# Optimization experiments

Measured on AMD Instinct MI355X. Metric: run time of the kernel, lower is better.

Reference implementation:

```python
import jax, jax.numpy as jnp
import numpy as np
from jax import lax

B, N, C = 4, 4096, 512
NUM_HEADS = 8
HD = C // NUM_HEADS  # 64, equals L
L = 64               # H = W = L, N = L*L


def setup_inputs() -> dict:
    key = jax.random.key(0)
    ks = jax.random.split(key, 8)
    d = HD
    return {
        "x": jax.random.normal(ks[0], (B, N, C), jnp.float32),
        "log_peak_width": jnp.log(jnp.float32(3.0)),
        "log_valley_width": jnp.log(jnp.float32(3.0)),
        "w_qkv": jax.random.normal(ks[1], (3 * C, C), jnp.float32) * 0.02,
        "b_qkv": jnp.zeros((3 * C,), jnp.float32),
        "w_proj": jax.random.normal(ks[2], (C, C), jnp.float32) * 0.02,
        "b_proj": jnp.zeros((C,), jnp.float32),
        "omega": jnp.linspace(0.1, 10.0, d // 2).astype(jnp.float32),
        "w_pp1": jax.random.normal(ks[3], (2 * d, 1, 3), jnp.float32) * 0.3,   # grouped conv, groups=d
        "b_pp1": jnp.zeros((2 * d,), jnp.float32),
        "w_pp2": jax.random.normal(ks[4], (d, 2 * d, 1), jnp.float32) * 0.1,
        "b_pp2": jnp.zeros((d,), jnp.float32),
        "w_gate": jax.random.normal(ks[5], (d, d, 1), jnp.float32) * 0.1,
        "b_gate": jnp.zeros((d,), jnp.float32),
    }


def _spectral_gate(x_spec, log_pw, log_vw):
    # x_spec: [B, C, N]. torch nonzero flattens (b,c,i) -> use per-position counts
    # (exactly equivalent to summing one gaussian per nonzero occurrence).
    n = x_spec.shape[-1]
    sc = jnp.sign(jnp.diff(jnp.diff(x_spec, axis=-1), axis=-1))       # [B,C,N-2]
    peak_cnt = jnp.sum(sc < 0, axis=(0, 1)).astype(x_spec.dtype)      # [N-2]
    valley_cnt = jnp.sum(sc > 0, axis=(0, 1)).astype(x_spec.dtype)    # [N-2]
    pos = jnp.arange(n, dtype=x_spec.dtype)
    centers = jnp.arange(1, n - 1, dtype=x_spec.dtype)                # index i+1

    def gsum(cnt, logw):
        dist = (pos[None, :] - centers[:, None]) * jnp.exp(-logw)     # [N-2, N]
        return cnt @ jnp.exp(-dist * dist)                            # [N]

    attn = gsum(peak_cnt, log_pw) + gsum(valley_cnt, log_vw)
    return (attn - attn.min()) / (attn.max() - attn.min() + 1e-6)     # [N], uniform over (B,C)


def _spectral_pe(omega, w1, b1, w2, b2, wg, bg, l, d):
    grid = jnp.arange(l, dtype=jnp.float32)
    rel = grid[:, None] - grid[None, :]                               # [l,l]
    freqs = rel[..., None] * omega                                    # [l,l,d/2]
    pe = jnp.concatenate([jnp.sin(freqs), jnp.cos(freqs)], axis=-1)   # [l,l,d]
    pe = pe.reshape(l * l, d).T[None]                                 # [1,d,l*l]
    dn = ('NCH', 'OIH', 'NCH')
    h = lax.conv_general_dilated(pe, w1, (1,), [(1, 1)], dimension_numbers=dn,
                                 feature_group_count=d) + b1[None, :, None]
    h = jax.nn.gelu(h, approximate=False)
    pe2 = (lax.conv_general_dilated(h, w2, (1,), [(0, 0)],
                                    dimension_numbers=dn) + b2[None, :, None])[0]  # [d, l*l]
    gate = jax.nn.sigmoid(wg[:, :, 0] @ pe2.mean(-1, keepdims=True) + bg[:, None])  # [d,1]
    pe3 = pe2.T.reshape(l, l, d)
    # torch rearrange '(l1 l2) d -> l1 l2 d' on [d,1] gate: reshape to [l, d//l, 1] and broadcast
    return pe3 * gate.reshape(l, d // l, 1)


def _rope(t, pe, d):
    b, h, n, _ = t.shape
    l = pe.shape[0]
    tr = t.reshape(b, h, l, l, d)
    tr = tr + tr * pe * (d ** -0.25)
    return tr.reshape(b, h, n, d)


def reference(x, log_peak_width, log_valley_width, w_qkv, b_qkv, w_proj, b_proj,
              omega, w_pp1, b_pp1, w_pp2, b_pp2, w_gate, b_gate):
    b, n, c = x.shape
    h, d = NUM_HEADS, HD
    gate = _spectral_gate(x.transpose(0, 2, 1), log_peak_width, log_valley_width)  # [n]
    xg = x * gate[None, :, None]
    qkv = xg @ w_qkv.T + b_qkv                                        # [b,n,3c]
    q, k, v = jnp.split(qkv, 3, axis=-1)
    tohead = lambda t: t.reshape(b, n, h, d).transpose(0, 2, 1, 3)    # [b,h,n,d]
    q, k, v = tohead(q), tohead(k), tohead(v)
    q = jax.nn.elu(q) + 1.0
    k = jax.nn.elu(k) + 1.0
    pe = _spectral_pe(omega, w_pp1, b_pp1, w_pp2, b_pp2, w_gate, b_gate, L, d)
    q = _rope(q, pe, d)
    k = _rope(k, pe, d)
    scale = (d * n) ** -0.5
    ctx = jnp.einsum('bhnd,bhne->bhde', q, k) * scale                 # [b,h,d,d]
    out = jnp.einsum('bhnd,bhde->bhne', v, ctx) * scale               # [b,h,n,d]
    out = out.transpose(0, 2, 1, 3).reshape(b, n, c)
    return out @ w_proj.T + b_proj
```

## Files before the change

kernel.cpp:

```cpp
#include <hip/hip_runtime.h>
#include <hip/hip_bf16.h>
#include <math.h>

constexpr int BB = 4;
constexpr int NN = 4096;
constexpr int CC = 512;
constexpr int HH = 8;
constexpr int DD = 64;
constexpr int NCNT = NN - 2;

typedef __bf16 bf16x8 __attribute__((ext_vector_type(8)));
typedef float f32x4 __attribute__((ext_vector_type(4)));

__device__ __forceinline__ float b2f(ushort u) {
  unsigned v = ((unsigned)u) << 16;
  return __builtin_bit_cast(float, v);
}
__device__ __forceinline__ ushort f2b(float f) {
  __hip_bfloat16 h = __float2bfloat16(f);
  return __builtin_bit_cast(ushort, h);
}
__device__ __forceinline__ void gload16(const ushort* g, ushort* l) {
  __builtin_amdgcn_global_load_lds(
      (const __attribute__((address_space(1))) unsigned int*)g,
      (__attribute__((address_space(3))) unsigned int*)l, 16, 0, 0);
}

__global__ __launch_bounds__(512) void k_counts_prep(
    const float* __restrict__ x, int* __restrict__ pcntP,
    int* __restrict__ pcntV, ushort* __restrict__ Xh) {
  int b = blockIdx.x >> 8;
  int tile = blockIdx.x & 255;
  int c = threadIdx.x;
  int lane = threadIdx.x & 63;
  int i0 = tile * 16;
  const float* xb = x + (size_t)b * NN * CC + c;

  float v[18];
  #pragma unroll
  for (int r = 0; r < 18; ++r) {
    int i = i0 + r;
    v[r] = xb[(size_t)(i < NN ? i : NN - 1) * CC];
  }

  #pragma unroll
  for (int r = 0; r < 16; ++r)
    Xh[((size_t)b * NN + i0 + r) * CC + c] = f2b(v[r]);

  __shared__ int redP[16], redV[16];
  if (threadIdx.x < 16) { redP[threadIdx.x] = 0; redV[threadIdx.x] = 0; }
  __syncthreads();

  #pragma unroll
  for (int r = 0; r < 16; ++r) {
    int i = i0 + r;
    if (i < NCNT) {
      float d2 = (v[r + 2] - v[r + 1]) - (v[r + 1] - v[r]);
      unsigned long long mneg = __ballot(d2 < 0.0f);
      unsigned long long mpos = __ballot(d2 > 0.0f);
      if (lane == 0) {
        atomicAdd(&redP[r], __popcll(mneg));
        atomicAdd(&redV[r], __popcll(mpos));
      }
    }
  }
  __syncthreads();
  if (threadIdx.x < 16) {
    int i = i0 + threadIdx.x;
    pcntP[b * NN + i] = (i < NCNT) ? redP[threadIdx.x] : 0;
    pcntV[b * NN + i] = (i < NCNT) ? redV[threadIdx.x] : 0;
  }
}

__global__ void k_etab2(const float* __restrict__ lpw, const float* __restrict__ lvw,
                        const int* __restrict__ pcntP, const int* __restrict__ pcntV,
                        float* __restrict__ etabP, float* __restrict__ etabV,
                        float* __restrict__ fcntP, float* __restrict__ fcntV) {
  int i = blockIdx.x * 256 + threadIdx.x;
  float ipw = expf(-lpw[0]);
  float ivw = expf(-lvw[0]);
  float t1 = (float)i * ipw;
  float t2 = (float)i * ivw;
  etabP[i] = expf(-t1 * t1);
  etabV[i] = expf(-t2 * t2);
  fcntP[i] = (float)(pcntP[i] + pcntP[NN + i] + pcntP[2 * NN + i] + pcntP[3 * NN + i]);
  fcntV[i] = (float)(pcntV[i] + pcntV[NN + i] + pcntV[2 * NN + i] + pcntV[3 * NN + i]);
}

__global__ void k_gsum(const float* __restrict__ fcntP, const float* __restrict__ fcntV,
                       const float* __restrict__ etabP, const float* __restrict__ etabV,
                       float* __restrict__ attn) {
  int p = blockIdx.x;
  int tid = threadIdx.x;
  float acc = 0.f;
  for (int i = tid; i < NCNT; i += 256) {
    int a = p - 1 - i;
    a = a < 0 ? -a : a;
    acc += fcntP[i] * etabP[a] + fcntV[i] * etabV[a];
  }
  __shared__ float red[256];
  red[tid] = acc;
  __syncthreads();
  for (int s = 128; s > 0; s >>= 1) {
    if (tid < s) red[tid] += red[tid + s];
    __syncthreads();
  }
  if (tid == 0) attn[p] = red[0];
}

__global__ void k_norm(const float* __restrict__ attn, float* __restrict__ gate) {
  int tid = threadIdx.x;
  float v0 = attn[tid], v1 = attn[tid + 1024], v2 = attn[tid + 2048], v3 = attn[tid + 3072];
  float mn = fminf(fminf(v0, v1), fminf(v2, v3));
  float mx = fmaxf(fmaxf(v0, v1), fmaxf(v2, v3));
  __shared__ float rmn[1024], rmx[1024];
  rmn[tid] = mn; rmx[tid] = mx;
  __syncthreads();
  for (int s = 512; s > 0; s >>= 1) {
    if (tid < s) {
      rmn[tid] = fminf(rmn[tid], rmn[tid + s]);
      rmx[tid] = fmaxf(rmx[tid], rmx[tid + s]);
    }
    __syncthreads();
  }
  float lo = rmn[0];
  float denom = rmx[0] - rmn[0] + 1e-6f;
  gate[tid]        = (v0 - lo) / denom;
  gate[tid + 1024] = (v1 - lo) / denom;
  gate[tid + 2048] = (v2 - lo) / denom;
  gate[tid + 3072] = (v3 - lo) / denom;
}

__global__ __launch_bounds__(256) void k_pe(
    const float* __restrict__ omega,
    const float* __restrict__ w1, const float* __restrict__ b1,
    const float* __restrict__ w2, const float* __restrict__ b2,
    float* __restrict__ pe2) {
  int g = threadIdx.x >> 6;
  int j = threadIdx.x & 63;
  int n = blockIdx.x * 4 + g;
  __shared__ float pec[4][3][64];
  __shared__ float hs[4][128];
  for (int t = 0; t < 3; ++t) {
    int m = n + t - 1;
    float v = 0.f;
    if (m >= 0 && m < NN) {
      int l1 = m >> 6, l2 = m & 63;
      float rel = (float)(l1 - l2);
      v = (j < 32) ? sinf(rel * omega[j]) : cosf(rel * omega[j - 32]);
    }
    pec[g][t][j] = v;
  }
  __syncthreads();
  for (int o = j; o < 128; o += 64) {
    int ci = o >> 1;
    float hv = b1[o];
    #pragma unroll
    for (int t = 0; t < 3; ++t) hv += pec[g][t][ci] * w1[o * 3 + t];
    hv = 0.5f * hv * (1.f + erff(hv * 0.70710678118654752f));
    hs[g][o] = hv;
  }
  __syncthreads();
  float acc = b2[j];
  for (int o = 0; o < 128; ++o) acc += hs[g][o] * w2[j * 128 + o];
  pe2[(size_t)j * NN + n] = acc;
}

__global__ void k_gatepe(const float* __restrict__ pe2,
                         const float* __restrict__ wg, const float* __restrict__ bg,
                         float* __restrict__ gpe) {
  int tid = threadIdx.x;
  int j = tid & 63, part = tid >> 6;
  float s = 0.f;
  const float* row = pe2 + (size_t)j * NN + part * 1024;
  for (int t = 0; t < 1024; ++t) s += row[t];
  __shared__ float ps[4][64];
  __shared__ float mean[64];
  ps[part][j] = s;
  __syncthreads();
  if (tid < 64) mean[j] = (ps[0][j] + ps[1][j] + ps[2][j] + ps[3][j]) * (1.f / 4096.f);
  __syncthreads();
  if (tid < 64) {
    float g = bg[j];
    for (int k2 = 0; k2 < 64; ++k2) g += wg[j * 64 + k2] * mean[k2];
    gpe[j] = 1.f / (1.f + expf(-g));
  }
}

__global__ void k_ropemul(const float* __restrict__ pe2, const float* __restrict__ gpe,
                          float* __restrict__ ropem) {
  int idx = blockIdx.x * 256 + threadIdx.x;
  int n = idx >> 6, dd = idx & 63;
  ropem[idx] = 1.f + pe2[(size_t)dd * NN + n] * gpe[n >> 6] * 0.35355339059327373f;
}

__global__ void k_prep_h(const float* __restrict__ src,
                         ushort* __restrict__ Sh, int nelem) {
  int idx4 = (blockIdx.x * 256 + threadIdx.x) * 4;
  if (idx4 >= nelem) return;
  float4 v = *(const float4*)&src[idx4];
  ushort4 h;
  ((ushort*)&h)[0] = f2b(v.x);
  ((ushort*)&h)[1] = f2b(v.y);
  ((ushort*)&h)[2] = f2b(v.z);
  ((ushort*)&h)[3] = f2b(v.w);
  *(ushort4*)&Sh[idx4] = h;
}

__global__ __launch_bounds__(256) void k_prep_wvt(const float* __restrict__ wqkv,
                                                  ushort* __restrict__ Wvth,
                                                  ushort* __restrict__ Wvtl) {
  int bx = blockIdx.x & 7;
  int by = blockIdx.x >> 3;
  __shared__ float t[64][65];
  int tid = threadIdx.x;
  #pragma unroll
  for (int it = 0; it < 4; ++it) {
    int idx = tid + it * 256;
    int r = idx >> 4;
    int c4 = (idx & 15) * 4;
    float4 v = *(const float4*)&wqkv[(size_t)(1024 + by * 64 + r) * 512 + bx * 64 + c4];
    t[r][c4] = v.x; t[r][c4 + 1] = v.y; t[r][c4 + 2] = v.z; t[r][c4 + 3] = v.w;
  }
  __syncthreads();
  #pragma unroll
  for (int it = 0; it < 4; ++it) {
    int idx = tid + it * 256;
    int r = idx >> 4;
    int c4 = (idx & 15) * 4;
    ushort4 h4, l4;
    #pragma unroll
    for (int q = 0; q < 4; ++q) {
      float v = t[c4 + q][r];
      ushort hi = f2b(v);
      ((ushort*)&h4)[q] = hi;
      ((ushort*)&l4)[q] = f2b(v - b2f(hi));
    }
    size_t o = (size_t)(bx * 64 + r) * 512 + by * 64 + c4;
    *(ushort4*)&Wvth[o] = h4;
    *(ushort4*)&Wvtl[o] = l4;
  }
}

template <int BN, int EPI>
__global__ __launch_bounds__(512) void k_gemm8(
    const ushort* __restrict__ Ag, const ushort* __restrict__ Bgh,
    const float* __restrict__ bias, const float* __restrict__ gate,
    const float* __restrict__ ropem,
    float* __restrict__ outF, ushort* __restrict__ qT, ushort* __restrict__ kT,
    int ntn, int ncols) {
  constexpr int NF = BN / 32;
  constexpr int BCH = BN / 16;
  const int nwg = gridDim.x;
  const int hw = blockIdx.x;
  const int logical = (hw & 7) * (nwg >> 3) + (hw >> 3);
  const int m0 = (logical / ntn) * 256, n0 = (logical % ntn) * BN;

  const int tid = threadIdx.x, wave = tid >> 6, lane = tid & 63;
  const int wm = wave >> 1, wn = wave & 1;
  __shared__ ushort sA[2][8192];
  __shared__ ushort sB[2][BN * 32];
  f32x4 acc[4][NF] = {};

  const int lr = lane >> 2;
  const int ci = lane & 3;
  const int scol = (ci ^ ((lr >> 1) & 3)) * 8;
  const int rA = lane & 15;
  const int cswz = ((lane >> 4) ^ ((rA >> 1) & 3)) * 8;

  const ushort* pA0 = Ag + (size_t)(m0 + (2 * wave) * 16 + lr) * CC + scol;
  const ushort* pA1 = Ag + (size_t)(m0 + (2 * wave + 1) * 16 + lr) * CC + scol;
  const ushort* Bh_ = Bgh + (EPI == 2 ? (size_t)(m0 >> 12) * 262144 : 0);
  const ushort* pB0 = Bh_ + (size_t)(n0 + wave * 16 + lr) * CC + scol;

#define STAGE(T, S)                                                        \
  {                                                                        \
    gload16(pA0 + (T) * 32, &sA[S][(2 * wave) * 512]);                     \
    gload16(pA1 + (T) * 32, &sA[S][(2 * wave + 1) * 512]);                 \
    if (BCH == 8) {                                                        \
      gload16(pB0 + (T) * 32, &sB[S][wave * 512]);                         \
    } else {                                                               \
      if (wave < BCH) gload16(pB0 + (T) * 32, &sB[S][wave * 512]);         \
    }                                                                      \
  }

  STAGE(0, 0);
  __syncthreads();

  #pragma unroll
  for (int t = 0; t < 16; ++t) {
    if (t < 15) STAGE(t + 1, (t + 1) & 1);
    const int cur = t & 1;
    bf16x8 af[4], bhf[NF];
    #pragma unroll
    for (int m = 0; m < 4; ++m)
      af[m] = *(const bf16x8*)(&sA[cur][(wm * 64 + m * 16 + rA) * 32 + cswz]);
    #pragma unroll
    for (int n = 0; n < NF; ++n)
      bhf[n] = *(const bf16x8*)(&sB[cur][(wn * (BN / 2) + n * 16 + rA) * 32 + cswz]);
    #pragma unroll
    for (int m = 0; m < 4; ++m)
      #pragma unroll
      for (int n = 0; n < NF; ++n)
        acc[m][n] = __builtin_amdgcn_mfma_f32_16x16x32_bf16(af[m], bhf[n], acc[m][n], 0, 0, 0);
    __syncthreads();
  }
#undef STAGE

  const int kj = lane >> 4, l15 = lane & 15;
  #pragma unroll
  for (int m = 0; m < 4; ++m) {
    #pragma unroll
    for (int n = 0; n < NF; ++n) {
      if (EPI == 2) {
        #pragma unroll
        for (int r = 0; r < 4; ++r) {
          int row = m0 + wm * 64 + m * 16 + kj * 4 + r;
          int col = n0 + wn * (BN / 2) + n * 16 + l15;
          int nseq = row & (NN - 1), b = row >> 12;
          float val = acc[m][n][r] * gate[nseq] + bias[b * 512 + col];
          outF[(size_t)row * ncols + col] = val;
        }
      } else {
        int rowb = m0 + wm * 64 + m * 16 + kj * 4;
        int col = n0 + wn * (BN / 2) + n * 16 + l15;
        int nseqb = rowb & (NN - 1), b = rowb >> 12;
        int part = col >> 9, h = (col >> 6) & 7, dd = col & 63;
        ushort4 pk;
        #pragma unroll
        for (int r = 0; r < 4; ++r) {
          int nseq = nseqb + r;
          float val = acc[m][n][r] * gate[nseq] + bias[col];
          float e = val > 0.f ? val + 1.f : expf(val);
          ((ushort*)&pk)[r] = f2b(e * ropem[nseq * 64 + dd]);
        }
        ushort* dst = (part == 0 ? qT : kT) +
                      ((size_t)(b * HH + h) * DD + dd) * NN + nseqb;
        *(ushort4*)dst = pk;
      }
    }
  }
}

__global__ __launch_bounds__(256) void k_gemm_g2(
    const ushort* __restrict__ Ag, const ushort* __restrict__ Bgh,
    const ushort* __restrict__ Bgl, ushort* __restrict__ outB, int ntn) {
  const int nwg = gridDim.x;
  const int hw = blockIdx.x;
  const int logical = (hw & 7) * (nwg >> 3) + (hw >> 3);
  const int m0 = (logical / ntn) * 128, n0 = (logical % ntn) * 128;

  const int tid = threadIdx.x, wave = tid >> 6, lane = tid & 63;
  const int wm = wave >> 1, wn = wave & 1;
  __shared__ ushort sA[2][4096];
  __shared__ ushort sB[2][8192];
  f32x4 acc[4][4] = {};

  const int lr = lane >> 2;
  const int ci = lane & 3;
  const int scol = (ci ^ ((lr >> 1) & 3)) * 8;
  const int rA = lane & 15;
  const int cswz = ((lane >> 4) ^ ((rA >> 1) & 3)) * 8;

  const int chunk0 = wave * 2, chunk1 = wave * 2 + 1;
  const ushort* pA0 = Ag + (size_t)(m0 + chunk0 * 16 + lr) * CC + scol;
  const ushort* pA1 = Ag + (size_t)(m0 + chunk1 * 16 + lr) * CC + scol;
  const ushort* pB0 = Bgh + (size_t)(n0 + chunk0 * 16 + lr) * CC + scol;
  const ushort* pB1 = Bgh + (size_t)(n0 + chunk1 * 16 + lr) * CC + scol;
  const ushort* pB0l = Bgl + (size_t)(n0 + chunk0 * 16 + lr) * CC + scol;
  const ushort* pB1l = Bgl + (size_t)(n0 + chunk1 * 16 + lr) * CC + scol;

#define STAGE(T, S)                                                        \
  {                                                                        \
    gload16(pA0 + (T) * 32, &sA[S][chunk0 * 512]);                         \
    gload16(pA1 + (T) * 32, &sA[S][chunk1 * 512]);                         \
    gload16(pB0 + (T) * 32, &sB[S][chunk0 * 512]);                         \
    gload16(pB1 + (T) * 32, &sB[S][chunk1 * 512]);                         \
    gload16(pB0l + (T) * 32, &sB[S][4096 + chunk0 * 512]);                 \
    gload16(pB1l + (T) * 32, &sB[S][4096 + chunk1 * 512]);                 \
  }

  STAGE(0, 0);
  __syncthreads();

  #pragma unroll
  for (int t = 0; t < 16; ++t) {
    if (t < 15) STAGE(t + 1, (t + 1) & 1);
    const int cur = t & 1;
    bf16x8 af[4], bh[4], bl[4];
    #pragma unroll
    for (int m = 0; m < 4; ++m)
      af[m] = *(const bf16x8*)(&sA[cur][(wm * 64 + m * 16 + rA) * 32 + cswz]);
    #pragma unroll
    for (int n = 0; n < 4; ++n) {
      int off = (wn * 64 + n * 16 + rA) * 32 + cswz;
      bh[n] = *(const bf16x8*)(&sB[cur][off]);
      bl[n] = *(const bf16x8*)(&sB[cur][4096 + off]);
    }
    #pragma unroll
    for (int m = 0; m < 4; ++m)
      #pragma unroll
      for (int n = 0; n < 4; ++n) {
        acc[m][n] = __builtin_amdgcn_mfma_f32_16x16x32_bf16(af[m], bh[n], acc[m][n], 0, 0, 0);
        acc[m][n] = __builtin_amdgcn_mfma_f32_16x16x32_bf16(af[m], bl[n], acc[m][n], 0, 0, 0);
      }
    __syncthreads();
  }
#undef STAGE

  const int kj = lane >> 4, l15 = lane & 15;
  #pragma unroll
  for (int m = 0; m < 4; ++m)
    #pragma unroll
    for (int n = 0; n < 4; ++n)
      #pragma unroll
      for (int r = 0; r < 4; ++r) {
        int row = m0 + wm * 64 + m * 16 + kj * 4 + r;
        int col = n0 + wn * 64 + n * 16 + l15;
        outB[(size_t)row * 512 + col] = f2b(acc[m][n][r]);
      }
}

__global__ __launch_bounds__(256) void k_ctx_mfma(
    const ushort* __restrict__ qT, const ushort* __restrict__ kT,
    float* __restrict__ ctxp) {
  int blk = blockIdx.x;
  int bh = blk >> 4, chunk = blk & 15;
  int wave = threadIdx.x >> 6, lane = threadIdx.x & 63;
  int l15 = lane & 15, kj = lane >> 4;
  const size_t base = (size_t)bh * DD * NN;
  const int n0 = chunk * 256 + wave * 64;
  f32x4 acc[4][4] = {};
  #pragma unroll
  for (int ks = 0; ks < 2; ++ks) {
    const int nb = n0 + ks * 32 + kj * 8;
    bf16x8 qa[4], ka[4];
    #pragma unroll
    for (int m = 0; m < 4; ++m)
      qa[m] = *(const bf16x8*)(qT + base + (size_t)(m * 16 + l15) * NN + nb);
    #pragma unroll
    for (int n = 0; n < 4; ++n)
      ka[n] = *(const bf16x8*)(kT + base + (size_t)(n * 16 + l15) * NN + nb);
    #pragma unroll
    for (int m = 0; m < 4; ++m)
      #pragma unroll
      for (int n = 0; n < 4; ++n)
        acc[m][n] = __builtin_amdgcn_mfma_f32_16x16x32_bf16(qa[m], ka[n], acc[m][n], 0, 0, 0);
  }
  __shared__ float red[4][4096];
  #pragma unroll
  for (int m = 0; m < 4; ++m)
    #pragma unroll
    for (int n = 0; n < 4; ++n)
      #pragma unroll
      for (int r = 0; r < 4; ++r)
        red[wave][(m * 16 + kj * 4 + r) * 64 + n * 16 + l15] = acc[m][n][r];
  __syncthreads();
  const float scale = 1.f / 512.f;
  float* dst = ctxp + (size_t)(bh * 16 + chunk) * 4096;
  #pragma unroll
  for (int e = 0; e < 16; ++e) {
    int idx = threadIdx.x + e * 256;
    float s = red[0][idx] + red[1][idx] + red[2][idx] + red[3][idx];
    dst[idx] = s * scale;
  }
}

__global__ void k_ctx_red(const float* __restrict__ ctxp, float* __restrict__ ctx) {
  int idx = blockIdx.x * 256 + threadIdx.x;
  int bh = idx >> 12, off = idx & 4095;
  float s = 0.f;
  #pragma unroll
  for (int c2 = 0; c2 < 16; ++c2)
    s += ctxp[((size_t)bh * 16 + c2) * 4096 + off];
  ctx[idx] = s;
}

__global__ __launch_bounds__(256) void k_mproj(
    const float* __restrict__ ctx, const float* __restrict__ wp,
    ushort* __restrict__ Mfh, ushort* __restrict__ Mfl) {
  int blk = blockIdx.x;
  int b = blk >> 6, h = (blk >> 3) & 7, oq = blk & 7;
  int tid = threadIdx.x;
  int o = oq * 64 + (tid & 63);
  int d0 = (tid >> 6) * 16;
  __shared__ float cs[64][64];
  #pragma unroll
  for (int it = 0; it < 4; ++it) {
    int idx = (tid + 256 * it) * 4;
    *(float4*)&cs[idx >> 6][idx & 63] =
        *(const float4*)&ctx[(size_t)(b * 8 + h) * 4096 + idx];
  }
  __syncthreads();
  float wv[64];
  #pragma unroll
  for (int e = 0; e < 64; ++e) wv[e] = wp[(size_t)o * 512 + h * 64 + e];
  for (int d = d0; d < d0 + 16; ++d) {
    float s = 0.f;
    #pragma unroll
    for (int e = 0; e < 64; ++e) s += cs[d][e] * wv[e];
    s *= (1.f / 512.f);
    ushort hi = f2b(s);
    size_t idx = ((size_t)b * 512 + o) * 512 + h * 64 + d;
    Mfh[idx] = hi;
    Mfl[idx] = f2b(s - b2f(hi));
  }
}

__global__ void k_beff(const ushort* __restrict__ Mfh, const ushort* __restrict__ Mfl,
                       const float* __restrict__ bqkv,
                       const float* __restrict__ bproj, float* __restrict__ beff) {
  int w = threadIdx.x >> 6, lane = threadIdx.x & 63;
  int t = blockIdx.x * 4 + w;
  int b = t >> 9, o = t & 511;
  size_t base = ((size_t)b * 512 + o) * 512;
  float s = 0.f;
  #pragma unroll
  for (int c = 0; c < 512; c += 64) {
    float m = b2f(Mfh[base + c + lane]) + b2f(Mfl[base + c + lane]);
    s += bqkv[1024 + c + lane] * m;
  }
  #pragma unroll
  for (int off = 32; off > 0; off >>= 1) s += __shfl_down(s, off);
  if (lane == 0) beff[t] = s + bproj[o];
}

extern "C" void kernel_launch(void* const* d_in, const int* in_sizes, int n_in,
                              void* d_out, int out_size, void* d_ws, size_t ws_size,
                              hipStream_t stream) {
  const float* x    = (const float*)d_in[0];
  const float* lpw  = (const float*)d_in[1];
  const float* lvw  = (const float*)d_in[2];
  const float* wqkv = (const float*)d_in[3];
  const float* bqkv = (const float*)d_in[4];
  const float* wproj= (const float*)d_in[5];
  const float* bproj= (const float*)d_in[6];
  const float* omega= (const float*)d_in[7];
  const float* w1   = (const float*)d_in[8];
  const float* b1   = (const float*)d_in[9];
  const float* w2   = (const float*)d_in[10];
  const float* b2   = (const float*)d_in[11];
  const float* wg   = (const float*)d_in[12];
  const float* bg   = (const float*)d_in[13];
  float* out = (float*)d_out;

  constexpr size_t MB = 1024 * 1024;
  char* w = (char*)d_ws;
  int*   pcntP  = (int*)(w);
  int*   pcntV  = (int*)(w + 64 * 1024);
  float* attn   = (float*)(w + 128 * 1024);
  float* gate   = (float*)(w + 144 * 1024);
  float* etabP  = (float*)(w + 160 * 1024);
  float* etabV  = (float*)(w + 176 * 1024);
  float* fcntP  = (float*)(w + 192 * 1024);
  float* fcntV  = (float*)(w + 208 * 1024);
  float* pe2    = (float*)(w + 256 * 1024);
  float* gpe    = (float*)(w + 1280 * 1024);
  float* ropem  = (float*)(w + 1344 * 1024);
  ushort* Xh    = (ushort*)(w + 4 * MB);
  ushort* qT    = (ushort*)(w + 20 * MB);
  ushort* kT    = (ushort*)(w + 36 * MB);
  ushort* Whqk  = (ushort*)(w + 52 * MB);
  ushort* Wvth  = (ushort*)(w + 53 * MB);
  ushort* Wvtl  = (ushort*)(w + 53 * MB + 512 * 1024);
  ushort* Mfh   = (ushort*)(w + 54 * MB);
  ushort* Mfl   = (ushort*)(w + 56 * MB);
  ushort* G2h   = (ushort*)(w + 58 * MB);
  float* beff   = (float*)(w + 60 * MB);
  float* ctxp   = (float*)(w + 61 * MB);
  float* ctx    = (float*)(w + 69 * MB);

  k_counts_prep<<<BB * 256, 512, 0, stream>>>(x, pcntP, pcntV, Xh);
  k_etab2<<<16, 256, 0, stream>>>(lpw, lvw, pcntP, pcntV, etabP, etabV, fcntP, fcntV);
  k_gsum<<<NN, 256, 0, stream>>>(fcntP, fcntV, etabP, etabV, attn);
  k_norm<<<1, 1024, 0, stream>>>(attn, gate);
  k_pe<<<1024, 256, 0, stream>>>(omega, w1, b1, w2, b2, pe2);
  k_gatepe<<<1, 256, 0, stream>>>(pe2, wg, bg, gpe);
  k_ropemul<<<1024, 256, 0, stream>>>(pe2, gpe, ropem);
  k_prep_h<<<512, 256, 0, stream>>>(wqkv, Whqk, 1024 * CC);
  k_prep_wvt<<<64, 256, 0, stream>>>(wqkv, Wvth, Wvtl);

  k_gemm8<128, 1><<<512, 512, 0, stream>>>(Xh, Whqk, bqkv, gate, ropem,
                                           nullptr, qT, kT, 8, 0);
  k_ctx_mfma<<<512, 256, 0, stream>>>(qT, kT, ctxp);
  k_ctx_red<<<512, 256, 0, stream>>>(ctxp, ctx);
  k_mproj<<<256, 256, 0, stream>>>(ctx, wproj, Mfh, Mfl);
  k_gemm_g2<<<64, 256, 0, stream>>>(Mfh, Wvth, Wvtl, G2h, 4);
  k_beff<<<512, 256, 0, stream>>>(Mfh, Mfl, bqkv, bproj, beff);

  k_gemm8<64, 2><<<512, 512, 0, stream>>>(Xh, G2h, beff, gate, nullptr,
                                          out, nullptr, nullptr, 8, 512);
}
```

Measured before the change: 178.7 us.

## Merge independent small kernels into block-dispatched combined launches

Independent preprocessing kernels (counts/bf16 cast, positional-encoding MLP, weight casts and transpose) are fused into one launch that dispatches on block index. The gate-table and PE-mean, the gsum and rope-multiplier, and the G2 GEMM and effective-bias kernels are likewise paired into shared launches. This cuts the launch count from 15 to 9, removing launch gaps and letting independent work run concurrently. In exchange the fused kernels share one register and LDS budget sized for the heaviest branch, which can reduce occupancy for the lighter branches.

```diff
diff --git a/kernel.cpp b/kernel.cpp
--- a/kernel.cpp
+++ b/kernel.cpp
@@ -26,86 +26,205 @@
       (__attribute__((address_space(3))) unsigned int*)l, 16, 0, 0);
 }
 
-__global__ __launch_bounds__(512) void k_counts_prep(
+__global__ __launch_bounds__(512) void k_front(
     const float* __restrict__ x, int* __restrict__ pcntP,
-    int* __restrict__ pcntV, ushort* __restrict__ Xh) {
-  int b = blockIdx.x >> 8;
-  int tile = blockIdx.x & 255;
-  int c = threadIdx.x;
-  int lane = threadIdx.x & 63;
-  int i0 = tile * 16;
-  const float* xb = x + (size_t)b * NN * CC + c;
-
-  float v[18];
-  #pragma unroll
-  for (int r = 0; r < 18; ++r) {
-    int i = i0 + r;
-    v[r] = xb[(size_t)(i < NN ? i : NN - 1) * CC];
-  }
-
-  #pragma unroll
-  for (int r = 0; r < 16; ++r)
-    Xh[((size_t)b * NN + i0 + r) * CC + c] = f2b(v[r]);
-
-  __shared__ int redP[16], redV[16];
-  if (threadIdx.x < 16) { redP[threadIdx.x] = 0; redV[threadIdx.x] = 0; }
-  __syncthreads();
-
-  #pragma unroll
-  for (int r = 0; r < 16; ++r) {
-    int i = i0 + r;
-    if (i < NCNT) {
-      float d2 = (v[r + 2] - v[r + 1]) - (v[r + 1] - v[r]);
-      unsigned long long mneg = __ballot(d2 < 0.0f);
-      unsigned long long mpos = __ballot(d2 > 0.0f);
-      if (lane == 0) {
-        atomicAdd(&redP[r], __popcll(mneg));
-        atomicAdd(&redV[r], __popcll(mpos));
+    int* __restrict__ pcntV, ushort* __restrict__ Xh,
+    const float* __restrict__ omega,
+    const float* __restrict__ w1, const float* __restrict__ b1,
+    const float* __restrict__ w2, const float* __restrict__ b2,
+    float* __restrict__ pe2,
+    const float* __restrict__ wqkv, ushort* __restrict__ Whqk,
+    ushort* __restrict__ Wvth, ushort* __restrict__ Wvtl) {
+  __shared__ __attribute__((aligned(16))) char sm[16896];
+  const int blk = blockIdx.x;
+  const int tid = threadIdx.x;
+
+  if (blk < 1024) {
+    int b = blk >> 8;
+    int tile = blk & 255;
+    int c = tid;
+    int lane = tid & 63;
+    int i0 = tile * 16;
+    const float* xb = x + (size_t)b * NN * CC + c;
+
+    float v[18];
+    #pragma unroll
+    for (int r = 0; r < 18; ++r) {
+      int i = i0 + r;
+      v[r] = xb[(size_t)(i < NN ? i : NN - 1) * CC];
+    }
+    #pragma unroll
+    for (int r = 0; r < 16; ++r)
+      Xh[((size_t)b * NN + i0 + r) * CC + c] = f2b(v[r]);
+
+    int* redP = (int*)sm;
+    int* redV = redP + 16;
+    if (tid < 16) { redP[tid] = 0; redV[tid] = 0; }
+    __syncthreads();
+    #pragma unroll
+    for (int r = 0; r < 16; ++r) {
+      int i = i0 + r;
+      if (i < NCNT) {
+        float d2 = (v[r + 2] - v[r + 1]) - (v[r + 1] - v[r]);
+        unsigned long long mneg = __ballot(d2 < 0.0f);
+        unsigned long long mpos = __ballot(d2 > 0.0f);
+        if (lane == 0) {
+          atomicAdd(&redP[r], __popcll(mneg));
+          atomicAdd(&redV[r], __popcll(mpos));
+        }
       }
     }
-  }
-  __syncthreads();
-  if (threadIdx.x < 16) {
-    int i = i0 + threadIdx.x;
-    pcntP[b * NN + i] = (i < NCNT) ? redP[threadIdx.x] : 0;
-    pcntV[b * NN + i] = (i < NCNT) ? redV[threadIdx.x] : 0;
-  }
-}
-
-__global__ void k_etab2(const float* __restrict__ lpw, const float* __restrict__ lvw,
-                        const int* __restrict__ pcntP, const int* __restrict__ pcntV,
-                        float* __restrict__ etabP, float* __restrict__ etabV,
-                        float* __restrict__ fcntP, float* __restrict__ fcntV) {
-  int i = blockIdx.x * 256 + threadIdx.x;
-  float ipw = expf(-lpw[0]);
-  float ivw = expf(-lvw[0]);
-  float t1 = (float)i * ipw;
-  float t2 = (float)i * ivw;
-  etabP[i] = expf(-t1 * t1);
-  etabV[i] = expf(-t2 * t2);
-  fcntP[i] = (float)(pcntP[i] + pcntP[NN + i] + pcntP[2 * NN + i] + pcntP[3 * NN + i]);
-  fcntV[i] = (float)(pcntV[i] + pcntV[NN + i] + pcntV[2 * NN + i] + pcntV[3 * NN + i]);
-}
-
-__global__ void k_gsum(const float* __restrict__ fcntP, const float* __restrict__ fcntV,
-                       const float* __restrict__ etabP, const float* __restrict__ etabV,
-                       float* __restrict__ attn) {
-  int p = blockIdx.x;
-  int tid = threadIdx.x;
-  float acc = 0.f;
-  for (int i = tid; i < NCNT; i += 256) {
-    int a = p - 1 - i;
-    a = a < 0 ? -a : a;
-    acc += fcntP[i] * etabP[a] + fcntV[i] * etabV[a];
-  }
-  __shared__ float red[256];
-  red[tid] = acc;
-  __syncthreads();
-  for (int s = 128; s > 0; s >>= 1) {
-    if (tid < s) red[tid] += red[tid + s];
-    __syncthreads();
-  }
-  if (tid == 0) attn[p] = red[0];
+    __syncthreads();
+    if (tid < 16) {
+      int i = i0 + tid;
+      pcntP[b * NN + i] = (i < NCNT) ? redP[tid] : 0;
+      pcntV[b * NN + i] = (i < NCNT) ? redV[tid] : 0;
+    }
+  } else if (blk < 1536) {
+    int pblk = blk - 1024;
+    int g = tid >> 6;
+    int j = tid & 63;
+    int n = pblk * 8 + g;
+    float (*pec)[3][64] = (float (*)[3][64])sm;
+    float (*hs)[128] = (float (*)[128])(sm + 6144);
+    for (int t = 0; t < 3; ++t) {
+      int m = n + t - 1;
+      float v = 0.f;
+      if (m >= 0 && m < NN) {
+        int l1 = m >> 6, l2 = m & 63;
+        float rel = (float)(l1 - l2);
+        v = (j < 32) ? sinf(rel * omega[j]) : cosf(rel * omega[j - 32]);
+      }
+      pec[g][t][j] = v;
+    }
+    __syncthreads();
+    for (int o = j; o < 128; o += 64) {
+      int ci = o >> 1;
+      float hv = b1[o];
+      #pragma unroll
+      for (int t = 0; t < 3; ++t) hv += pec[g][t][ci] * w1[o * 3 + t];
+      hv = 0.5f * hv * (1.f + erff(hv * 0.70710678118654752f));
+      hs[g][o] = hv;
+    }
+    __syncthreads();
+    float acc = b2[j];
+    for (int o = 0; o < 128; ++o) acc += hs[g][o] * w2[j * 128 + o];
+    pe2[(size_t)j * NN + n] = acc;
+  } else if (blk < 1792) {
+    int hblk = blk - 1536;
+    int idx4 = (hblk * 512 + tid) * 4;
+    float4 v = *(const float4*)&wqkv[idx4];
+    ushort4 h;
+    ((ushort*)&h)[0] = f2b(v.x);
+    ((ushort*)&h)[1] = f2b(v.y);
+    ((ushort*)&h)[2] = f2b(v.z);
+    ((ushort*)&h)[3] = f2b(v.w);
+    *(ushort4*)&Whqk[idx4] = h;
+  } else {
+    int wblk = blk - 1792;
+    int bx = wblk & 7;
+    int by = wblk >> 3;
+    float (*t)[65] = (float (*)[65])sm;
+    if (tid < 256) {
+      #pragma unroll
+      for (int it = 0; it < 4; ++it) {
+        int idx = tid + it * 256;
+        int r = idx >> 4;
+        int c4 = (idx & 15) * 4;
+        float4 v = *(const float4*)&wqkv[(size_t)(1024 + by * 64 + r) * 512 + bx * 64 + c4];
+        t[r][c4] = v.x; t[r][c4 + 1] = v.y; t[r][c4 + 2] = v.z; t[r][c4 + 3] = v.w;
+      }
+    }
+    __syncthreads();
+    if (tid < 256) {
+      #pragma unroll
+      for (int it = 0; it < 4; ++it) {
+        int idx = tid + it * 256;
+        int r = idx >> 4;
+        int c4 = (idx & 15) * 4;
+        ushort4 h4, l4;
+        #pragma unroll
+        for (int q = 0; q < 4; ++q) {
+          float v = t[c4 + q][r];
+          ushort hi = f2b(v);
+          ((ushort*)&h4)[q] = hi;
+          ((ushort*)&l4)[q] = f2b(v - b2f(hi));
+        }
+        size_t o = (size_t)(bx * 64 + r) * 512 + by * 64 + c4;
+        *(ushort4*)&Wvth[o] = h4;
+        *(ushort4*)&Wvtl[o] = l4;
+      }
+    }
+  }
+}
+
+__global__ __launch_bounds__(256) void k_mid1(
+    const float* __restrict__ lpw, const float* __restrict__ lvw,
+    const int* __restrict__ pcntP, const int* __restrict__ pcntV,
+    float* __restrict__ etabP, float* __restrict__ etabV,
+    float* __restrict__ fcntP, float* __restrict__ fcntV,
+    const float* __restrict__ pe2, const float* __restrict__ wg,
+    const float* __restrict__ bg, float* __restrict__ gpe) {
+  const int blk = blockIdx.x;
+  const int tid = threadIdx.x;
+  if (blk < 16) {
+    int i = blk * 256 + tid;
+    float ipw = expf(-lpw[0]);
+    float ivw = expf(-lvw[0]);
+    float t1 = (float)i * ipw;
+    float t2 = (float)i * ivw;
+    etabP[i] = expf(-t1 * t1);
+    etabV[i] = expf(-t2 * t2);
+    fcntP[i] = (float)(pcntP[i] + pcntP[NN + i] + pcntP[2 * NN + i] + pcntP[3 * NN + i]);
+    fcntV[i] = (float)(pcntV[i] + pcntV[NN + i] + pcntV[2 * NN + i] + pcntV[3 * NN + i]);
+  } else {
+    int j = tid & 63, part = tid >> 6;
+    float s = 0.f;
+    const float* row = pe2 + (size_t)j * NN + part * 1024;
+    for (int t = 0; t < 1024; ++t) s += row[t];
+    __shared__ float ps[4][64];
+    __shared__ float mean[64];
+    ps[part][j] = s;
+    __syncthreads();
+    if (tid < 64) mean[j] = (ps[0][j] + ps[1][j] + ps[2][j] + ps[3][j]) * (1.f / 4096.f);
+    __syncthreads();
+    if (tid < 64) {
+      float g = bg[j];
+      for (int k2 = 0; k2 < 64; ++k2) g += wg[j * 64 + k2] * mean[k2];
+      gpe[j] = 1.f / (1.f + expf(-g));
+    }
+  }
+}
+
+__global__ __launch_bounds__(256) void k_mid2(
+    const float* __restrict__ fcntP, const float* __restrict__ fcntV,
+    const float* __restrict__ etabP, const float* __restrict__ etabV,
+    float* __restrict__ attn,
+    const float* __restrict__ pe2, const float* __restrict__ gpe,
+    float* __restrict__ ropem) {
+  const int blk = blockIdx.x;
+  const int tid = threadIdx.x;
+  if (blk < 4096) {
+    int p = blk;
+    float acc = 0.f;
+    for (int i = tid; i < NCNT; i += 256) {
+      int a = p - 1 - i;
+      a = a < 0 ? -a : a;
+      acc += fcntP[i] * etabP[a] + fcntV[i] * etabV[a];
+    }
+    __shared__ float red[256];
+    red[tid] = acc;
+    __syncthreads();
+    for (int s = 128; s > 0; s >>= 1) {
+      if (tid < s) red[tid] += red[tid + s];
+      __syncthreads();
+    }
+    if (tid == 0) attn[p] = red[0];
+  } else {
+    int idx = (blk - 4096) * 256 + tid;
+    int n = idx >> 6, dd = idx & 63;
+    ropem[idx] = 1.f + pe2[(size_t)dd * NN + n] * gpe[n >> 6] * 0.35355339059327373f;
+  }
 }
 
 __global__ void k_norm(const float* __restrict__ attn, float* __restrict__ gate) {
@@ -129,117 +248,6 @@
   gate[tid + 1024] = (v1 - lo) / denom;
   gate[tid + 2048] = (v2 - lo) / denom;
   gate[tid + 3072] = (v3 - lo) / denom;
-}
-
-__global__ __launch_bounds__(256) void k_pe(
-    const float* __restrict__ omega,
-    const float* __restrict__ w1, const float* __restrict__ b1,
-    const float* __restrict__ w2, const float* __restrict__ b2,
-    float* __restrict__ pe2) {
-  int g = threadIdx.x >> 6;
-  int j = threadIdx.x & 63;
-  int n = blockIdx.x * 4 + g;
-  __shared__ float pec[4][3][64];
-  __shared__ float hs[4][128];
-  for (int t = 0; t < 3; ++t) {
-    int m = n + t - 1;
-    float v = 0.f;
-    if (m >= 0 && m < NN) {
-      int l1 = m >> 6, l2 = m & 63;
-      float rel = (float)(l1 - l2);
-      v = (j < 32) ? sinf(rel * omega[j]) : cosf(rel * omega[j - 32]);
-    }
-    pec[g][t][j] = v;
-  }
-  __syncthreads();
-  for (int o = j; o < 128; o += 64) {
-    int ci = o >> 1;
-    float hv = b1[o];
-    #pragma unroll
-    for (int t = 0; t < 3; ++t) hv += pec[g][t][ci] * w1[o * 3 + t];
-    hv = 0.5f * hv * (1.f + erff(hv * 0.70710678118654752f));
-    hs[g][o] = hv;
-  }
-  __syncthreads();
-  float acc = b2[j];
-  for (int o = 0; o < 128; ++o) acc += hs[g][o] * w2[j * 128 + o];
-  pe2[(size_t)j * NN + n] = acc;
-}
-
-__global__ void k_gatepe(const float* __restrict__ pe2,
-                         const float* __restrict__ wg, const float* __restrict__ bg,
-                         float* __restrict__ gpe) {
-  int tid = threadIdx.x;
-  int j = tid & 63, part = tid >> 6;
-  float s = 0.f;
-  const float* row = pe2 + (size_t)j * NN + part * 1024;
-  for (int t = 0; t < 1024; ++t) s += row[t];
-  __shared__ float ps[4][64];
-  __shared__ float mean[64];
-  ps[part][j] = s;
-  __syncthreads();
-  if (tid < 64) mean[j] = (ps[0][j] + ps[1][j] + ps[2][j] + ps[3][j]) * (1.f / 4096.f);
-  __syncthreads();
-  if (tid < 64) {
-    float g = bg[j];
-    for (int k2 = 0; k2 < 64; ++k2) g += wg[j * 64 + k2] * mean[k2];
-    gpe[j] = 1.f / (1.f + expf(-g));
-  }
-}
-
-__global__ void k_ropemul(const float* __restrict__ pe2, const float* __restrict__ gpe,
-                          float* __restrict__ ropem) {
-  int idx = blockIdx.x * 256 + threadIdx.x;
-  int n = idx >> 6, dd = idx & 63;
-  ropem[idx] = 1.f + pe2[(size_t)dd * NN + n] * gpe[n >> 6] * 0.35355339059327373f;
-}
-
-__global__ void k_prep_h(const float* __restrict__ src,
-                         ushort* __restrict__ Sh, int nelem) {
-  int idx4 = (blockIdx.x * 256 + threadIdx.x) * 4;
-  if (idx4 >= nelem) return;
-  float4 v = *(const float4*)&src[idx4];
-  ushort4 h;
-  ((ushort*)&h)[0] = f2b(v.x);
-  ((ushort*)&h)[1] = f2b(v.y);
-  ((ushort*)&h)[2] = f2b(v.z);
-  ((ushort*)&h)[3] = f2b(v.w);
-  *(ushort4*)&Sh[idx4] = h;
-}
-
-__global__ __launch_bounds__(256) void k_prep_wvt(const float* __restrict__ wqkv,
-                                                  ushort* __restrict__ Wvth,
-                                                  ushort* __restrict__ Wvtl) {
-  int bx = blockIdx.x & 7;
-  int by = blockIdx.x >> 3;
-  __shared__ float t[64][65];
-  int tid = threadIdx.x;
-  #pragma unroll
-  for (int it = 0; it < 4; ++it) {
-    int idx = tid + it * 256;
-    int r = idx >> 4;
-    int c4 = (idx & 15) * 4;
-    float4 v = *(const float4*)&wqkv[(size_t)(1024 + by * 64 + r) * 512 + bx * 64 + c4];
-    t[r][c4] = v.x; t[r][c4 + 1] = v.y; t[r][c4 + 2] = v.z; t[r][c4 + 3] = v.w;
-  }
-  __syncthreads();
-  #pragma unroll
-  for (int it = 0; it < 4; ++it) {
-    int idx = tid + it * 256;
-    int r = idx >> 4;
-    int c4 = (idx & 15) * 4;
-    ushort4 h4, l4;
-    #pragma unroll
-    for (int q = 0; q < 4; ++q) {
-      float v = t[c4 + q][r];
-      ushort hi = f2b(v);
-      ((ushort*)&h4)[q] = hi;
-      ((ushort*)&l4)[q] = f2b(v - b2f(hi));
-    }
-    size_t o = (size_t)(bx * 64 + r) * 512 + by * 64 + c4;
-    *(ushort4*)&Wvth[o] = h4;
-    *(ushort4*)&Wvtl[o] = l4;
-  }
 }
 
 template <int BN, int EPI>
@@ -342,85 +350,6 @@
   }
 }
 
-__global__ __launch_bounds__(256) void k_gemm_g2(
-    const ushort* __restrict__ Ag, const ushort* __restrict__ Bgh,
-    const ushort* __restrict__ Bgl, ushort* __restrict__ outB, int ntn) {
-  const int nwg = gridDim.x;
-  const int hw = blockIdx.x;
-  const int logical = (hw & 7) * (nwg >> 3) + (hw >> 3);
-  const int m0 = (logical / ntn) * 128, n0 = (logical % ntn) * 128;
-
-  const int tid = threadIdx.x, wave = tid >> 6, lane = tid & 63;
-  const int wm = wave >> 1, wn = wave & 1;
-  __shared__ ushort sA[2][4096];
-  __shared__ ushort sB[2][8192];
-  f32x4 acc[4][4] = {};
-
-  const int lr = lane >> 2;
-  const int ci = lane & 3;
-  const int scol = (ci ^ ((lr >> 1) & 3)) * 8;
-  const int rA = lane & 15;
-  const int cswz = ((lane >> 4) ^ ((rA >> 1) & 3)) * 8;
-
-  const int chunk0 = wave * 2, chunk1 = wave * 2 + 1;
-  const ushort* pA0 = Ag + (size_t)(m0 + chunk0 * 16 + lr) * CC + scol;
-  const ushort* pA1 = Ag + (size_t)(m0 + chunk1 * 16 + lr) * CC + scol;
-  const ushort* pB0 = Bgh + (size_t)(n0 + chunk0 * 16 + lr) * CC + scol;
-  const ushort* pB1 = Bgh + (size_t)(n0 + chunk1 * 16 + lr) * CC + scol;
-  const ushort* pB0l = Bgl + (size_t)(n0 + chunk0 * 16 + lr) * CC + scol;
-  const ushort* pB1l = Bgl + (size_t)(n0 + chunk1 * 16 + lr) * CC + scol;
-
-#define STAGE(T, S)                                                        \
-  {                                                                        \
-    gload16(pA0 + (T) * 32, &sA[S][chunk0 * 512]);                         \
-    gload16(pA1 + (T) * 32, &sA[S][chunk1 * 512]);                         \
-    gload16(pB0 + (T) * 32, &sB[S][chunk0 * 512]);                         \
-    gload16(pB1 + (T) * 32, &sB[S][chunk1 * 512]);                         \
-    gload16(pB0l + (T) * 32, &sB[S][4096 + chunk0 * 512]);                 \
-    gload16(pB1l + (T) * 32, &sB[S][4096 + chunk1 * 512]);                 \
-  }
-
-  STAGE(0, 0);
-  __syncthreads();
-
-  #pragma unroll
-  for (int t = 0; t < 16; ++t) {
-    if (t < 15) STAGE(t + 1, (t + 1) & 1);
-    const int cur = t & 1;
-    bf16x8 af[4], bh[4], bl[4];
-    #pragma unroll
-    for (int m = 0; m < 4; ++m)
-      af[m] = *(const bf16x8*)(&sA[cur][(wm * 64 + m * 16 + rA) * 32 + cswz]);
-    #pragma unroll
-    for (int n = 0; n < 4; ++n) {
-      int off = (wn * 64 + n * 16 + rA) * 32 + cswz;
-      bh[n] = *(const bf16x8*)(&sB[cur][off]);
-      bl[n] = *(const bf16x8*)(&sB[cur][4096 + off]);
-    }
-    #pragma unroll
-    for (int m = 0; m < 4; ++m)
-      #pragma unroll
-      for (int n = 0; n < 4; ++n) {
-        acc[m][n] = __builtin_amdgcn_mfma_f32_16x16x32_bf16(af[m], bh[n], acc[m][n], 0, 0, 0);
-        acc[m][n] = __builtin_amdgcn_mfma_f32_16x16x32_bf16(af[m], bl[n], acc[m][n], 0, 0, 0);
-      }
-    __syncthreads();
-  }
-#undef STAGE
-
-  const int kj = lane >> 4, l15 = lane & 15;
-  #pragma unroll
-  for (int m = 0; m < 4; ++m)
-    #pragma unroll
-    for (int n = 0; n < 4; ++n)
-      #pragma unroll
-      for (int r = 0; r < 4; ++r) {
-        int row = m0 + wm * 64 + m * 16 + kj * 4 + r;
-        int col = n0 + wn * 64 + n * 16 + l15;
-        outB[(size_t)row * 512 + col] = f2b(acc[m][n][r]);
-      }
-}
-
 __global__ __launch_bounds__(256) void k_ctx_mfma(
     const ushort* __restrict__ qT, const ushort* __restrict__ kT,
     float* __restrict__ ctxp) {
@@ -507,22 +436,99 @@
   }
 }
 
-__global__ void k_beff(const ushort* __restrict__ Mfh, const ushort* __restrict__ Mfl,
-                       const float* __restrict__ bqkv,
-                       const float* __restrict__ bproj, float* __restrict__ beff) {
-  int w = threadIdx.x >> 6, lane = threadIdx.x & 63;
-  int t = blockIdx.x * 4 + w;
-  int b = t >> 9, o = t & 511;
-  size_t base = ((size_t)b * 512 + o) * 512;
-  float s = 0.f;
-  #pragma unroll
-  for (int c = 0; c < 512; c += 64) {
-    float m = b2f(Mfh[base + c + lane]) + b2f(Mfl[base + c + lane]);
-    s += bqkv[1024 + c + lane] * m;
-  }
-  #pragma unroll
-  for (int off = 32; off > 0; off >>= 1) s += __shfl_down(s, off);
-  if (lane == 0) beff[t] = s + bproj[o];
+__global__ __launch_bounds__(256) void k_tail(
+    const ushort* __restrict__ Mfh, const ushort* __restrict__ Mfl,
+    const ushort* __restrict__ Wvth, const ushort* __restrict__ Wvtl,
+    ushort* __restrict__ G2h,
+    const float* __restrict__ bqkv, const float* __restrict__ bproj,
+    float* __restrict__ beff) {
+  const int blk = blockIdx.x;
+  if (blk < 64) {
+    const int logical = (blk & 7) * 8 + (blk >> 3);
+    const int m0 = (logical / 4) * 128, n0 = (logical % 4) * 128;
+    const int tid = threadIdx.x, wave = tid >> 6, lane = tid & 63;
+    const int wm = wave >> 1, wn = wave & 1;
+    __shared__ ushort sA[2][4096];
+    __shared__ ushort sB[2][8192];
+    f32x4 acc[4][4] = {};
+
+    const int lr = lane >> 2;
+    const int ci = lane & 3;
+    const int scol = (ci ^ ((lr >> 1) & 3)) * 8;
+    const int rA = lane & 15;
+    const int cswz = ((lane >> 4) ^ ((rA >> 1) & 3)) * 8;
+
+    const int chunk0 = wave * 2, chunk1 = wave * 2 + 1;
+    const ushort* pA0 = Mfh + (size_t)(m0 + chunk0 * 16 + lr) * CC + scol;
+    const ushort* pA1 = Mfh + (size_t)(m0 + chunk1 * 16 + lr) * CC + scol;
+    const ushort* pB0 = Wvth + (size_t)(n0 + chunk0 * 16 + lr) * CC + scol;
+    const ushort* pB1 = Wvth + (size_t)(n0 + chunk1 * 16 + lr) * CC + scol;
+    const ushort* pB0l = Wvtl + (size_t)(n0 + chunk0 * 16 + lr) * CC + scol;
+    const ushort* pB1l = Wvtl + (size_t)(n0 + chunk1 * 16 + lr) * CC + scol;
+
+#define STAGE(T, S)                                                        \
+    {                                                                      \
+      gload16(pA0 + (T) * 32, &sA[S][chunk0 * 512]);                       \
+      gload16(pA1 + (T) * 32, &sA[S][chunk1 * 512]);                       \
+      gload16(pB0 + (T) * 32, &sB[S][chunk0 * 512]);                       \
+      gload16(pB1 + (T) * 32, &sB[S][chunk1 * 512]);                       \
+      gload16(pB0l + (T) * 32, &sB[S][4096 + chunk0 * 512]);               \
+      gload16(pB1l + (T) * 32, &sB[S][4096 + chunk1 * 512]);               \
+    }
+
+    STAGE(0, 0);
+    __syncthreads();
+    #pragma unroll
+    for (int t = 0; t < 16; ++t) {
+      if (t < 15) STAGE(t + 1, (t + 1) & 1);
+      const int cur = t & 1;
+      bf16x8 af[4], bh[4], bl[4];
+      #pragma unroll
+      for (int m = 0; m < 4; ++m)
+        af[m] = *(const bf16x8*)(&sA[cur][(wm * 64 + m * 16 + rA) * 32 + cswz]);
+      #pragma unroll
+      for (int n = 0; n < 4; ++n) {
+        int off = (wn * 64 + n * 16 + rA) * 32 + cswz;
+        bh[n] = *(const bf16x8*)(&sB[cur][off]);
+        bl[n] = *(const bf16x8*)(&sB[cur][4096 + off]);
+      }
+      #pragma unroll
+      for (int m = 0; m < 4; ++m)
+        #pragma unroll
+        for (int n = 0; n < 4; ++n) {
+          acc[m][n] = __builtin_amdgcn_mfma_f32_16x16x32_bf16(af[m], bh[n], acc[m][n], 0, 0, 0);
+          acc[m][n] = __builtin_amdgcn_mfma_f32_16x16x32_bf16(af[m], bl[n], acc[m][n], 0, 0, 0);
+        }
+      __syncthreads();
+    }
+#undef STAGE
+
+    const int kj = lane >> 4, l15 = lane & 15;
+    #pragma unroll
+    for (int m = 0; m < 4; ++m)
+      #pragma unroll
+      for (int n = 0; n < 4; ++n)
+        #pragma unroll
+        for (int r = 0; r < 4; ++r) {
+          int row = m0 + wm * 64 + m * 16 + kj * 4 + r;
+          int col = n0 + wn * 64 + n * 16 + l15;
+          G2h[(size_t)row * 512 + col] = f2b(acc[m][n][r]);
+        }
+  } else {
+    int w = threadIdx.x >> 6, lane = threadIdx.x & 63;
+    int t = (blk - 64) * 4 + w;
+    int b = t >> 9, o = t & 511;
+    size_t base = ((size_t)b * 512 + o) * 512;
+    float s = 0.f;
+    #pragma unroll
+    for (int c = 0; c < 512; c += 64) {
+      float m = b2f(Mfh[base + c + lane]) + b2f(Mfl[base + c + lane]);
+      s += bqkv[1024 + c + lane] * m;
+    }
+    #pragma unroll
+    for (int off = 32; off > 0; off >>= 1) s += __shfl_down(s, off);
+    if (lane == 0) beff[t] = s + bproj[o];
+  }
 }
 
 extern "C" void kernel_launch(void* const* d_in, const int* in_sizes, int n_in,
@@ -570,23 +576,20 @@
   float* ctxp   = (float*)(w + 61 * MB);
   float* ctx    = (float*)(w + 69 * MB);
 
-  k_counts_prep<<<BB * 256, 512, 0, stream>>>(x, pcntP, pcntV, Xh);
-  k_etab2<<<16, 256, 0, stream>>>(lpw, lvw, pcntP, pcntV, etabP, etabV, fcntP, fcntV);
-  k_gsum<<<NN, 256, 0, stream>>>(fcntP, fcntV, etabP, etabV, attn);
+  k_front<<<1856, 512, 0, stream>>>(x, pcntP, pcntV, Xh, omega, w1, b1, w2, b2,
+                                    pe2, wqkv, Whqk, Wvth, Wvtl);
+  k_mid1<<<17, 256, 0, stream>>>(lpw, lvw, pcntP, pcntV, etabP, etabV,
+                                 fcntP, fcntV, pe2, wg, bg, gpe);
+  k_mid2<<<5120, 256, 0, stream>>>(fcntP, fcntV, etabP, etabV, attn,
+                                   pe2, gpe, ropem);
   k_norm<<<1, 1024, 0, stream>>>(attn, gate);
-  k_pe<<<1024, 256, 0, stream>>>(omega, w1, b1, w2, b2, pe2);
-  k_gatepe<<<1, 256, 0, stream>>>(pe2, wg, bg, gpe);
-  k_ropemul<<<1024, 256, 0, stream>>>(pe2, gpe, ropem);
-  k_prep_h<<<512, 256, 0, stream>>>(wqkv, Whqk, 1024 * CC);
-  k_prep_wvt<<<64, 256, 0, stream>>>(wqkv, Wvth, Wvtl);
 
   k_gemm8<128, 1><<<512, 512, 0, stream>>>(Xh, Whqk, bqkv, gate, ropem,
                                            nullptr, qT, kT, 8, 0);
   k_ctx_mfma<<<512, 256, 0, stream>>>(qT, kT, ctxp);
   k_ctx_red<<<512, 256, 0, stream>>>(ctxp, ctx);
   k_mproj<<<256, 256, 0, stream>>>(ctx, wproj, Mfh, Mfl);
-  k_gemm_g2<<<64, 256, 0, stream>>>(Mfh, Wvth, Wvtl, G2h, 4);
-  k_beff<<<512, 256, 0, stream>>>(Mfh, Mfl, bqkv, bproj, beff);
+  k_tail<<<576, 256, 0, stream>>>(Mfh, Mfl, Wvth, Wvtl, G2h, bqkv, bproj, beff);
 
   k_gemm8<64, 2><<<512, 512, 0, stream>>>(Xh, G2h, beff, gate, nullptr,
                                           out, nullptr, nullptr, 8, 512);
```

Measured after the change: 169.3 us. 1.06x faster.
